# Performance work log

Measured on AMD Instinct MI355X. Metric: run time of the kernel, lower is better.

The kernel has to match this reference:

```python
import jax, jax.numpy as jnp
import numpy as np

QF = 28  # quality_factor from init

_BASE_QUANT = np.array([
    [16, 11, 10, 16, 24, 40, 51, 61],
    [12, 12, 14, 19, 26, 58, 60, 55],
    [14, 13, 16, 24, 40, 57, 69, 56],
    [14, 17, 22, 29, 51, 87, 80, 62],
    [18, 22, 37, 56, 68, 109, 103, 77],
    [24, 35, 55, 64, 81, 104, 113, 92],
    [49, 64, 78, 87, 103, 121, 120, 101],
    [72, 92, 95, 98, 112, 100, 103, 99]], dtype=np.float32)

def _quant_matrix(qf: int) -> jnp.ndarray:
    scale = 50.0 / max(1, qf) if qf < 25 else 200.0 - 2 * qf
    return jnp.asarray(np.maximum(_BASE_QUANT * scale / 50.0, 1.0), dtype=jnp.float32)

def _dct_basis(N: int = 8) -> jnp.ndarray:
    # Orthonormal DCT-II basis: basis @ x @ basis.T is the 2D DCT (norm='ortho')
    k = np.arange(N)[:, None].astype(np.float32)
    n = np.arange(N)[None, :].astype(np.float32)
    b = np.sqrt(2.0 / N) * np.cos(np.pi * k * (2 * n + 1) / (2 * N))
    b[0, :] = np.sqrt(1.0 / N)
    return jnp.asarray(b, dtype=jnp.float32)

def setup_inputs() -> dict:
    key = jax.random.key(0)
    x = jax.random.uniform(key, (8, 3, 1080, 1920), dtype=jnp.float32) * 255.0
    return {"x": x}

def reference(x):
    B, C, H, W = x.shape
    basis = _dct_basis(8)
    q = _quant_matrix(QF)  # (8, 8)

    # BGR -> Y (luminance)
    b, g, r = x[:, 0:1], x[:, 1:2], x[:, 2:3]
    y = 0.114 * b + 0.587 * g + 0.299 * r  # (B, 1, H, W)

    # pad to multiple of 8 (replicate)
    pad_h, pad_w = (-H) % 8, (-W) % 8
    yp = jnp.pad(y, ((0, 0), (0, 0), (0, pad_h), (0, pad_w)), mode='edge') if (pad_h or pad_w) else y
    Hp, Wp = H + pad_h, W + pad_w
    nh, nw = Hp // 8, Wp // 8

    # split into 8x8 blocks: (B, 1, nh, nw, 8, 8)
    blocks = yp.reshape(B, 1, nh, 8, nw, 8).transpose(0, 1, 2, 4, 3, 5)

    # 2D DCT (ortho): basis @ block @ basis.T
    coef = jnp.einsum('ki,...ij,lj->...kl', basis, blocks, basis)

    # hard quantization with straight-through estimator (training-mode forward == hard)
    qhard = jnp.round(coef / (q + 1e-8)) * q
    coef_q = coef + jax.lax.stop_gradient(qhard - coef)

    # 2D inverse DCT: basis.T @ block @ basis
    rec = jnp.einsum('ik,...ij,jl->...kl', basis, coef_q, basis)

    # reassemble blocks -> image, crop padding
    y_rec = rec.transpose(0, 1, 2, 4, 3, 5).reshape(B, 1, Hp, Wp)[:, :, :H, :W]

    # Y back to BGR: add luminance delta weighted by the BGR->Y coefficients
    yd = y_rec - y
    out = jnp.concatenate([b + 0.114 * yd, g + 0.587 * yd, r + 0.299 * yd], axis=1)
    return jnp.clip(out, 0.0, 255.0)
```

## Files before the change

### kernel.cpp

```cpp
#include <hip/hip_runtime.h>
#include <math.h>

#define IMG_H 1080
#define IMG_W 1920
#define HW (IMG_H * IMG_W)
#define NBATCH 8

typedef float f4 __attribute__((ext_vector_type(4)));

__device__ __constant__ int BASEQ[64] = {
    16, 11, 10, 16, 24, 40, 51, 61,
    12, 12, 14, 19, 26, 58, 60, 55,
    14, 13, 16, 24, 40, 57, 69, 56,
    14, 17, 22, 29, 51, 87, 80, 62,
    18, 22, 37, 56, 68, 109, 103, 77,
    24, 35, 55, 64, 81, 104, 113, 92,
    49, 64, 78, 87, 103, 121, 120, 101,
    72, 92, 95, 98, 112, 100, 103, 99};

__device__ __forceinline__ float clamp255(float v) {
    return fminf(fmaxf(v, 0.0f), 255.0f);
}

__device__ __forceinline__ void wave_lds_fence() {
    __builtin_amdgcn_wave_barrier();
    __builtin_amdgcn_s_waitcnt(0xC07F);
    __builtin_amdgcn_wave_barrier();
}

__global__ __launch_bounds__(192) void h264_kernel(const float* __restrict__ x,
                                                   float* __restrict__ out) {
    __shared__ __align__(16) float yt[3 * 512];
    __shared__ float t2[3 * 576];
    __shared__ float bl[64];
    __shared__ float ql[64];

    const int t = threadIdx.x;
    const int wave = t >> 6;
    const int lane = t & 63;

    {
        int k = lane >> 3, n = lane & 7;
        float v;
        if (k == 0) {
            v = 0.35355339059327373f;
        } else {
            float a = 3.14159265358979323846f * (float)k;
            a = a * (2.0f * (float)n + 1.0f);
            a = a / 16.0f;
            v = 0.5f * cosf(a);
        }
        bl[lane] = v;
        ql[lane] = __fdiv_rn((float)(BASEQ[lane] * 144), 50.0f);
    }

    const int h0 = blockIdx.y * 8;
    const int wcol0 = blockIdx.x * 192 + wave * 64;
    const int bat = blockIdx.z;
    const float* xb = x + (size_t)bat * 3 * HW;
    float* ob = out + (size_t)bat * 3 * HW;

    float* ytw = yt + wave * 512;
    float* t2w = t2 + wave * 576;

    f4 Bv[2], Gv[2], Rv[2];
    int gaddr[2];
#pragma unroll
    for (int it = 0; it < 2; ++it) {
        int idx = lane + (it << 6);
        int row = idx >> 4;
        int c4 = (idx & 15) << 2;
        int ga = (h0 + row) * IMG_W + wcol0 + c4;
        gaddr[it] = ga;
        Bv[it] = __builtin_nontemporal_load((const f4*)(xb + ga));
        Gv[it] = __builtin_nontemporal_load((const f4*)(xb + HW + ga));
        Rv[it] = __builtin_nontemporal_load((const f4*)(xb + 2 * HW + ga));
        f4 y4;
        y4.x = __fadd_rn(__fadd_rn(__fmul_rn(0.114f, Bv[it].x), __fmul_rn(0.587f, Gv[it].x)), __fmul_rn(0.299f, Rv[it].x));
        y4.y = __fadd_rn(__fadd_rn(__fmul_rn(0.114f, Bv[it].y), __fmul_rn(0.587f, Gv[it].y)), __fmul_rn(0.299f, Rv[it].y));
        y4.z = __fadd_rn(__fadd_rn(__fmul_rn(0.114f, Bv[it].z), __fmul_rn(0.587f, Gv[it].z)), __fmul_rn(0.299f, Rv[it].z));
        y4.w = __fadd_rn(__fadd_rn(__fmul_rn(0.114f, Bv[it].w), __fmul_rn(0.587f, Gv[it].w)), __fmul_rn(0.299f, Rv[it].w));
        *(f4*)(ytw + row * 64 + c4) = y4;
    }
    wave_lds_fence();

    const int blk = lane >> 3;
    const int l = lane & 7;
    float* t2b = t2w + blk * 72;

    float ycol[8];
#pragma unroll
    for (int i = 0; i < 8; ++i) ycol[i] = ytw[i * 64 + lane];

    float c1[8];
#pragma unroll
    for (int k = 0; k < 8; ++k) {
        float acc = 0.0f;
#pragma unroll
        for (int i = 0; i < 8; ++i) acc = fmaf(bl[k * 8 + i], ycol[i], acc);
        c1[k] = acc;
    }
#pragma unroll
    for (int k = 0; k < 8; ++k) t2b[l * 9 + k] = c1[k];
    wave_lds_fence();

    float coef[8];
#pragma unroll
    for (int k = 0; k < 8; ++k) {
        float acc = 0.0f;
#pragma unroll
        for (int j = 0; j < 8; ++j) acc = fmaf(t2b[j * 9 + k], bl[l * 8 + j], acc);
        float q = ql[k * 8 + l];
        coef[k] = __fmul_rn(rintf(__fdiv_rn(acc, q)), q);
    }
    wave_lds_fence();
#pragma unroll
    for (int k = 0; k < 8; ++k) t2b[l * 9 + k] = coef[k];
    wave_lds_fence();

    float s[8];
#pragma unroll
    for (int i = 0; i < 8; ++i) {
        float acc = 0.0f;
#pragma unroll
        for (int j = 0; j < 8; ++j) acc = fmaf(t2b[j * 9 + i], bl[j * 8 + l], acc);
        s[i] = acc;
    }
    float yd[8];
#pragma unroll
    for (int k = 0; k < 8; ++k) {
        float acc = 0.0f;
#pragma unroll
        for (int i = 0; i < 8; ++i) acc = fmaf(bl[i * 8 + k], s[i], acc);
        yd[k] = __fsub_rn(acc, ycol[k]);
    }
#pragma unroll
    for (int k = 0; k < 8; ++k) ytw[k * 64 + lane] = yd[k];
    wave_lds_fence();

#pragma unroll
    for (int it = 0; it < 2; ++it) {
        int idx = lane + (it << 6);
        int row = idx >> 4;
        int c4 = (idx & 15) << 2;
        f4 y4 = *(f4*)(ytw + row * 64 + c4);
        int ga = gaddr[it];
        f4 o0, o1, o2;
        o0.x = clamp255(__fadd_rn(Bv[it].x, __fmul_rn(0.114f, y4.x)));
        o0.y = clamp255(__fadd_rn(Bv[it].y, __fmul_rn(0.114f, y4.y)));
        o0.z = clamp255(__fadd_rn(Bv[it].z, __fmul_rn(0.114f, y4.z)));
        o0.w = clamp255(__fadd_rn(Bv[it].w, __fmul_rn(0.114f, y4.w)));
        o1.x = clamp255(__fadd_rn(Gv[it].x, __fmul_rn(0.587f, y4.x)));
        o1.y = clamp255(__fadd_rn(Gv[it].y, __fmul_rn(0.587f, y4.y)));
        o1.z = clamp255(__fadd_rn(Gv[it].z, __fmul_rn(0.587f, y4.z)));
        o1.w = clamp255(__fadd_rn(Gv[it].w, __fmul_rn(0.587f, y4.w)));
        o2.x = clamp255(__fadd_rn(Rv[it].x, __fmul_rn(0.299f, y4.x)));
        o2.y = clamp255(__fadd_rn(Rv[it].y, __fmul_rn(0.299f, y4.y)));
        o2.z = clamp255(__fadd_rn(Rv[it].z, __fmul_rn(0.299f, y4.z)));
        o2.w = clamp255(__fadd_rn(Rv[it].w, __fmul_rn(0.299f, y4.w)));
        __builtin_nontemporal_store(o0, (f4*)(ob + ga));
        __builtin_nontemporal_store(o1, (f4*)(ob + HW + ga));
        __builtin_nontemporal_store(o2, (f4*)(ob + 2 * HW + ga));
    }
}

extern "C" void kernel_launch(void* const* d_in, const int* in_sizes, int n_in,
                              void* d_out, int out_size, void* d_ws, size_t ws_size,
                              hipStream_t stream) {
    const float* x = (const float*)d_in[0];
    float* out = (float*)d_out;
    dim3 grid(IMG_W / 192, IMG_H / 8, NBATCH);
    dim3 block(192);
    h264_kernel<<<grid, block, 0, stream>>>(x, out);
}
```

Baseline: 316.0 us.

## Process two columns per lane with packed FP32 math and readlane basis

Each wave now covers 128 columns instead of 64, so every lane handles two columns and the grid is halved. The DCT/IDCT, colour conversion and clamp use packed two-wide FMA (v_pk_fma_f32). Basis coefficients come from readlane broadcasts and pre-packed LDS tables instead of scalar LDS reads. Quantization divides via a reciprocal plus one Newton correction step. The goal is less per-element ALU and LDS-instruction overhead in what may be a compute-bound kernel, at the cost of more registers, more LDS, fewer blocks, and a risk of rounding differences in the quantization step.

```diff
diff --git a/kernel.cpp b/kernel.cpp
--- a/kernel.cpp
+++ b/kernel.cpp
@@ -7,6 +7,7 @@
 #define NBATCH 8
 
 typedef float f4 __attribute__((ext_vector_type(4)));
+typedef float f2 __attribute__((ext_vector_type(2)));
 
 __device__ __constant__ int BASEQ[64] = {
     16, 11, 10, 16, 24, 40, 51, 61,
@@ -18,30 +19,43 @@
     49, 64, 78, 87, 103, 121, 120, 101,
     72, 92, 95, 98, 112, 100, 103, 99};
 
-__device__ __forceinline__ float clamp255(float v) {
-    return fminf(fmaxf(v, 0.0f), 255.0f);
-}
-
 __device__ __forceinline__ void wave_lds_fence() {
     __builtin_amdgcn_wave_barrier();
     __builtin_amdgcn_s_waitcnt(0xC07F);
     __builtin_amdgcn_wave_barrier();
 }
 
+__device__ __forceinline__ f2 splat2(float s) { f2 r = {s, s}; return r; }
+__device__ __forceinline__ f2 pk_fma(f2 a, f2 b, f2 c) { return __builtin_elementwise_fma(a, b, c); }
+__device__ __forceinline__ f2 mul_nofuse(float c, f2 x) {
+    f2 z = {0.0f, 0.0f};
+    return __builtin_elementwise_fma(splat2(c), x, z);
+}
+__device__ __forceinline__ float uread(float v, int idx) {
+    return __uint_as_float(__builtin_amdgcn_readlane(__float_as_uint(v), idx));
+}
+__device__ __forceinline__ f2 clamp2(f2 x) {
+    f2 lo = {0.0f, 0.0f}, hi = {255.0f, 255.0f};
+    return __builtin_elementwise_min(__builtin_elementwise_max(x, lo), hi);
+}
+
 __global__ __launch_bounds__(192) void h264_kernel(const float* __restrict__ x,
                                                    float* __restrict__ out) {
-    __shared__ __align__(16) float yt[3 * 512];
-    __shared__ float t2[3 * 576];
-    __shared__ float bl[64];
-    __shared__ float ql[64];
+    __shared__ __align__(16) float yt[3 * 1024];
+    __shared__ __align__(16) float t2[3 * 1600];
+    __shared__ __align__(16) float blRM[64];
+    __shared__ __align__(16) f2 PB[32];
+    __shared__ __align__(16) f2 PBc[32];
+    __shared__ __align__(16) f2 QP[32];
+    __shared__ __align__(16) f2 RP[32];
 
     const int t = threadIdx.x;
     const int wave = t >> 6;
     const int lane = t & 63;
 
+    float v;
     {
         int k = lane >> 3, n = lane & 7;
-        float v;
         if (k == 0) {
             v = 0.35355339059327373f;
         } else {
@@ -50,117 +64,186 @@
             a = a / 16.0f;
             v = 0.5f * cosf(a);
         }
-        bl[lane] = v;
-        ql[lane] = __fdiv_rn((float)(BASEQ[lane] * 144), 50.0f);
-    }
+        blRM[lane] = v;
+    }
+    wave_lds_fence();
+    {
+        int e = lane & 31;
+        int j = e >> 3, m = e & 7;
+        if (lane < 32) {
+            f2 pbv = {blRM[16 * j + m], blRM[16 * j + 8 + m]};
+            PB[e] = pbv;
+            float qa = __fdiv_rn((float)(BASEQ[m * 8 + 2 * j] * 144), 50.0f);
+            float qb = __fdiv_rn((float)(BASEQ[m * 8 + 2 * j + 1] * 144), 50.0f);
+            f2 qv = {qa, qb};
+            f2 rv = {__fdiv_rn(1.0f, qa), __fdiv_rn(1.0f, qb)};
+            QP[e] = qv;
+            RP[e] = rv;
+        } else {
+            f2 pcv = {blRM[m * 8 + 2 * j], blRM[m * 8 + 2 * j + 1]};
+            PBc[e] = pcv;
+        }
+    }
+    wave_lds_fence();
 
     const int h0 = blockIdx.y * 8;
-    const int wcol0 = blockIdx.x * 192 + wave * 64;
-    const int bat = blockIdx.z;
-    const float* xb = x + (size_t)bat * 3 * HW;
-    float* ob = out + (size_t)bat * 3 * HW;
-
-    float* ytw = yt + wave * 512;
-    float* t2w = t2 + wave * 576;
-
-    f4 Bv[2], Gv[2], Rv[2];
-    int gaddr[2];
-#pragma unroll
-    for (int it = 0; it < 2; ++it) {
+    const int wcol0 = blockIdx.x * 384 + wave * 128;
+    const float* xb = x + (size_t)blockIdx.z * 3 * HW;
+    float* ob = out + (size_t)blockIdx.z * 3 * HW;
+    float* ytw = yt + wave * 1024;
+    float* t2w = t2 + wave * 1600;
+
+    f4 Bv[4], Gv[4], Rv[4];
+    int gaddr[4];
+#pragma unroll
+    for (int it = 0; it < 4; ++it) {
         int idx = lane + (it << 6);
-        int row = idx >> 4;
-        int c4 = (idx & 15) << 2;
+        int row = idx >> 5;
+        int c4 = (idx & 31) << 2;
         int ga = (h0 + row) * IMG_W + wcol0 + c4;
         gaddr[it] = ga;
         Bv[it] = __builtin_nontemporal_load((const f4*)(xb + ga));
         Gv[it] = __builtin_nontemporal_load((const f4*)(xb + HW + ga));
         Rv[it] = __builtin_nontemporal_load((const f4*)(xb + 2 * HW + ga));
-        f4 y4;
-        y4.x = __fadd_rn(__fadd_rn(__fmul_rn(0.114f, Bv[it].x), __fmul_rn(0.587f, Gv[it].x)), __fmul_rn(0.299f, Rv[it].x));
-        y4.y = __fadd_rn(__fadd_rn(__fmul_rn(0.114f, Bv[it].y), __fmul_rn(0.587f, Gv[it].y)), __fmul_rn(0.299f, Rv[it].y));
-        y4.z = __fadd_rn(__fadd_rn(__fmul_rn(0.114f, Bv[it].z), __fmul_rn(0.587f, Gv[it].z)), __fmul_rn(0.299f, Rv[it].z));
-        y4.w = __fadd_rn(__fadd_rn(__fmul_rn(0.114f, Bv[it].w), __fmul_rn(0.587f, Gv[it].w)), __fmul_rn(0.299f, Rv[it].w));
-        *(f4*)(ytw + row * 64 + c4) = y4;
-    }
-    wave_lds_fence();
-
-    const int blk = lane >> 3;
-    const int l = lane & 7;
-    float* t2b = t2w + blk * 72;
-
-    float ycol[8];
-#pragma unroll
-    for (int i = 0; i < 8; ++i) ycol[i] = ytw[i * 64 + lane];
-
-    float c1[8];
-#pragma unroll
-    for (int k = 0; k < 8; ++k) {
-        float acc = 0.0f;
-#pragma unroll
-        for (int i = 0; i < 8; ++i) acc = fmaf(bl[k * 8 + i], ycol[i], acc);
-        c1[k] = acc;
-    }
-#pragma unroll
-    for (int k = 0; k < 8; ++k) t2b[l * 9 + k] = c1[k];
-    wave_lds_fence();
-
-    float coef[8];
-#pragma unroll
-    for (int k = 0; k < 8; ++k) {
-        float acc = 0.0f;
-#pragma unroll
-        for (int j = 0; j < 8; ++j) acc = fmaf(t2b[j * 9 + k], bl[l * 8 + j], acc);
-        float q = ql[k * 8 + l];
-        coef[k] = __fmul_rn(rintf(__fdiv_rn(acc, q)), q);
-    }
-    wave_lds_fence();
-#pragma unroll
-    for (int k = 0; k < 8; ++k) t2b[l * 9 + k] = coef[k];
-    wave_lds_fence();
-
-    float s[8];
+    }
+#pragma unroll
+    for (int it = 0; it < 4; ++it) {
+        f2 b_l = {Bv[it].x, Bv[it].y}, b_h = {Bv[it].z, Bv[it].w};
+        f2 g_l = {Gv[it].x, Gv[it].y}, g_h = {Gv[it].z, Gv[it].w};
+        f2 r_l = {Rv[it].x, Rv[it].y}, r_h = {Rv[it].z, Rv[it].w};
+        f2 ylo = (mul_nofuse(0.114f, b_l) + mul_nofuse(0.587f, g_l)) + mul_nofuse(0.299f, r_l);
+        f2 yhi = (mul_nofuse(0.114f, b_h) + mul_nofuse(0.587f, g_h)) + mul_nofuse(0.299f, r_h);
+        int idx = lane + (it << 6);
+        int row = idx >> 5;
+        int c4 = (idx & 31) << 2;
+        f4 y4 = {ylo.x, ylo.y, yhi.x, yhi.y};
+        *(f4*)(ytw + row * 128 + c4) = y4;
+    }
+    wave_lds_fence();
+
+    const int blk = lane >> 2;
+    const int j = lane & 3;
+    float* t2b = t2w + blk * 100;
+
+    f2 y2c[8];
+#pragma unroll
+    for (int i = 0; i < 8; ++i) y2c[i] = *(const f2*)(ytw + i * 128 + 2 * lane);
+
+#pragma unroll
+    for (int k = 0; k < 8; ++k) {
+        f2 acc = {0.0f, 0.0f};
+#pragma unroll
+        for (int i = 0; i < 8; ++i) acc = pk_fma(splat2(uread(v, 8 * k + i)), y2c[i], acc);
+        *(f2*)(t2b + k * 12 + 2 * j) = acc;
+    }
+    wave_lds_fence();
+
+    f2 pb[8];
+    {
+        const f4* p = (const f4*)(PB + 8 * j);
+        f4 a0 = p[0], a1 = p[1], a2 = p[2], a3 = p[3];
+        pb[0] = f2{a0.x, a0.y}; pb[1] = f2{a0.z, a0.w};
+        pb[2] = f2{a1.x, a1.y}; pb[3] = f2{a1.z, a1.w};
+        pb[4] = f2{a2.x, a2.y}; pb[5] = f2{a2.z, a2.w};
+        pb[6] = f2{a3.x, a3.y}; pb[7] = f2{a3.z, a3.w};
+    }
+    f2 acc2[8];
+#pragma unroll
+    for (int k = 0; k < 8; ++k) {
+        f4 ta = *(const f4*)(t2b + k * 12);
+        f4 tb = *(const f4*)(t2b + k * 12 + 4);
+        f2 acc = {0.0f, 0.0f};
+        acc = pk_fma(splat2(ta.x), pb[0], acc);
+        acc = pk_fma(splat2(ta.y), pb[1], acc);
+        acc = pk_fma(splat2(ta.z), pb[2], acc);
+        acc = pk_fma(splat2(ta.w), pb[3], acc);
+        acc = pk_fma(splat2(tb.x), pb[4], acc);
+        acc = pk_fma(splat2(tb.y), pb[5], acc);
+        acc = pk_fma(splat2(tb.z), pb[6], acc);
+        acc = pk_fma(splat2(tb.w), pb[7], acc);
+        acc2[k] = acc;
+    }
+    wave_lds_fence();
+    f2 qp_[8], rp_[8];
+    {
+        const f4* pq = (const f4*)(QP + 8 * j);
+        const f4* pr = (const f4*)(RP + 8 * j);
+        f4 a0 = pq[0], a1 = pq[1], a2 = pq[2], a3 = pq[3];
+        qp_[0] = f2{a0.x, a0.y}; qp_[1] = f2{a0.z, a0.w};
+        qp_[2] = f2{a1.x, a1.y}; qp_[3] = f2{a1.z, a1.w};
+        qp_[4] = f2{a2.x, a2.y}; qp_[5] = f2{a2.z, a2.w};
+        qp_[6] = f2{a3.x, a3.y}; qp_[7] = f2{a3.z, a3.w};
+        f4 b0 = pr[0], b1 = pr[1], b2 = pr[2], b3 = pr[3];
+        rp_[0] = f2{b0.x, b0.y}; rp_[1] = f2{b0.z, b0.w};
+        rp_[2] = f2{b1.x, b1.y}; rp_[3] = f2{b1.z, b1.w};
+        rp_[4] = f2{b2.x, b2.y}; rp_[5] = f2{b2.z, b2.w};
+        rp_[6] = f2{b3.x, b3.y}; rp_[7] = f2{b3.z, b3.w};
+    }
+#pragma unroll
+    for (int k = 0; k < 8; ++k) {
+        f2 acc = acc2[k];
+        f2 q0 = acc * rp_[k];
+        f2 e = pk_fma(-qp_[k], q0, acc);
+        f2 q1 = pk_fma(e, rp_[k], q0);
+        f2 n = {rintf(q1.x), rintf(q1.y)};
+        f2 c = n * qp_[k];
+        *(f2*)(t2b + k * 12 + 2 * j) = c;
+    }
+    wave_lds_fence();
+
+    f2 pbc[8];
+    {
+        const f4* p = (const f4*)(PBc + 8 * j);
+        f4 a0 = p[0], a1 = p[1], a2 = p[2], a3 = p[3];
+        pbc[0] = f2{a0.x, a0.y}; pbc[1] = f2{a0.z, a0.w};
+        pbc[2] = f2{a1.x, a1.y}; pbc[3] = f2{a1.z, a1.w};
+        pbc[4] = f2{a2.x, a2.y}; pbc[5] = f2{a2.z, a2.w};
+        pbc[6] = f2{a3.x, a3.y}; pbc[7] = f2{a3.z, a3.w};
+    }
+    f2 s2[8];
 #pragma unroll
     for (int i = 0; i < 8; ++i) {
-        float acc = 0.0f;
-#pragma unroll
-        for (int j = 0; j < 8; ++j) acc = fmaf(t2b[j * 9 + i], bl[j * 8 + l], acc);
-        s[i] = acc;
-    }
-    float yd[8];
-#pragma unroll
-    for (int k = 0; k < 8; ++k) {
-        float acc = 0.0f;
-#pragma unroll
-        for (int i = 0; i < 8; ++i) acc = fmaf(bl[i * 8 + k], s[i], acc);
-        yd[k] = __fsub_rn(acc, ycol[k]);
-    }
-#pragma unroll
-    for (int k = 0; k < 8; ++k) ytw[k * 64 + lane] = yd[k];
-    wave_lds_fence();
-
-#pragma unroll
-    for (int it = 0; it < 2; ++it) {
+        f4 ca = *(const f4*)(t2b + i * 12);
+        f4 cb = *(const f4*)(t2b + i * 12 + 4);
+        f2 acc = {0.0f, 0.0f};
+        acc = pk_fma(splat2(ca.x), pbc[0], acc);
+        acc = pk_fma(splat2(ca.y), pbc[1], acc);
+        acc = pk_fma(splat2(ca.z), pbc[2], acc);
+        acc = pk_fma(splat2(ca.w), pbc[3], acc);
+        acc = pk_fma(splat2(cb.x), pbc[4], acc);
+        acc = pk_fma(splat2(cb.y), pbc[5], acc);
+        acc = pk_fma(splat2(cb.z), pbc[6], acc);
+        acc = pk_fma(splat2(cb.w), pbc[7], acc);
+        s2[i] = acc;
+    }
+#pragma unroll
+    for (int k = 0; k < 8; ++k) {
+        f2 acc = {0.0f, 0.0f};
+#pragma unroll
+        for (int i = 0; i < 8; ++i) acc = pk_fma(splat2(uread(v, 8 * i + k)), s2[i], acc);
+        f2 yd = acc - y2c[k];
+        *(f2*)(ytw + k * 128 + 2 * lane) = yd;
+    }
+    wave_lds_fence();
+
+#pragma unroll
+    for (int it = 0; it < 4; ++it) {
         int idx = lane + (it << 6);
-        int row = idx >> 4;
-        int c4 = (idx & 15) << 2;
-        f4 y4 = *(f4*)(ytw + row * 64 + c4);
+        int row = idx >> 5;
+        int c4 = (idx & 31) << 2;
+        f4 y4 = *(const f4*)(ytw + row * 128 + c4);
+        f2 ylo = {y4.x, y4.y}, yhi = {y4.z, y4.w};
         int ga = gaddr[it];
-        f4 o0, o1, o2;
-        o0.x = clamp255(__fadd_rn(Bv[it].x, __fmul_rn(0.114f, y4.x)));
-        o0.y = clamp255(__fadd_rn(Bv[it].y, __fmul_rn(0.114f, y4.y)));
-        o0.z = clamp255(__fadd_rn(Bv[it].z, __fmul_rn(0.114f, y4.z)));
-        o0.w = clamp255(__fadd_rn(Bv[it].w, __fmul_rn(0.114f, y4.w)));
-        o1.x = clamp255(__fadd_rn(Gv[it].x, __fmul_rn(0.587f, y4.x)));
-        o1.y = clamp255(__fadd_rn(Gv[it].y, __fmul_rn(0.587f, y4.y)));
-        o1.z = clamp255(__fadd_rn(Gv[it].z, __fmul_rn(0.587f, y4.z)));
-        o1.w = clamp255(__fadd_rn(Gv[it].w, __fmul_rn(0.587f, y4.w)));
-        o2.x = clamp255(__fadd_rn(Rv[it].x, __fmul_rn(0.299f, y4.x)));
-        o2.y = clamp255(__fadd_rn(Rv[it].y, __fmul_rn(0.299f, y4.y)));
-        o2.z = clamp255(__fadd_rn(Rv[it].z, __fmul_rn(0.299f, y4.z)));
-        o2.w = clamp255(__fadd_rn(Rv[it].w, __fmul_rn(0.299f, y4.w)));
-        __builtin_nontemporal_store(o0, (f4*)(ob + ga));
-        __builtin_nontemporal_store(o1, (f4*)(ob + HW + ga));
-        __builtin_nontemporal_store(o2, (f4*)(ob + 2 * HW + ga));
+        f2 t0, t1v;
+        t0 = clamp2(f2{Bv[it].x, Bv[it].y} + mul_nofuse(0.114f, ylo));
+        t1v = clamp2(f2{Bv[it].z, Bv[it].w} + mul_nofuse(0.114f, yhi));
+        __builtin_nontemporal_store(f4{t0.x, t0.y, t1v.x, t1v.y}, (f4*)(ob + ga));
+        t0 = clamp2(f2{Gv[it].x, Gv[it].y} + mul_nofuse(0.587f, ylo));
+        t1v = clamp2(f2{Gv[it].z, Gv[it].w} + mul_nofuse(0.587f, yhi));
+        __builtin_nontemporal_store(f4{t0.x, t0.y, t1v.x, t1v.y}, (f4*)(ob + HW + ga));
+        t0 = clamp2(f2{Rv[it].x, Rv[it].y} + mul_nofuse(0.299f, ylo));
+        t1v = clamp2(f2{Rv[it].z, Rv[it].w} + mul_nofuse(0.299f, yhi));
+        __builtin_nontemporal_store(f4{t0.x, t0.y, t1v.x, t1v.y}, (f4*)(ob + 2 * HW + ga));
     }
 }
 
@@ -169,7 +252,7 @@
                               hipStream_t stream) {
     const float* x = (const float*)d_in[0];
     float* out = (float*)d_out;
-    dim3 grid(IMG_W / 192, IMG_H / 8, NBATCH);
+    dim3 grid(IMG_W / 384, IMG_H / 8, NBATCH);
     dim3 block(192);
     h264_kernel<<<grid, block, 0, stream>>>(x, out);
 }
```

After: 319.1 us. Within noise of the previous version (+1.0%).
